# Optimization experiments

Hardware: AMD Instinct MI355X
Metric: run time of the kernel (lower is better)

Reference implementation:

```python
import jax, jax.numpy as jnp
import numpy as np

B, IN, H = 8192, 512, 512


def _binarize(w):
    # sign() forward with straight-through gradient (ebnn Binarize)
    return w + jax.lax.stop_gradient(jnp.sign(w) - w)


def setup_inputs() -> dict:
    key = jax.random.key(0)
    ks = jax.random.split(key, 7)
    stdv = 1.0 / np.sqrt(H)
    return {
        "x": jax.random.normal(ks[0], (B, IN), jnp.float32),
        "hx": jax.random.normal(ks[1], (B, H), jnp.float32),
        "cx": jax.random.normal(ks[2], (B, H), jnp.float32),
        "W_ih": jax.random.uniform(ks[3], (4 * H, IN), jnp.float32, -stdv, stdv),
        "W_hh": jax.random.uniform(ks[4], (4 * H, H), jnp.float32, -stdv, stdv),
        "bias_ih": jax.random.uniform(ks[5], (4 * H,), jnp.float32, -stdv, stdv),
        "bias_hh": jax.random.uniform(ks[6], (4 * H,), jnp.float32, -stdv, stdv),
    }


def reference(x, hx, cx, W_ih, W_hh, bias_ih, bias_hh):
    # gates: [B, 4H] = x @ sign(W_ih)^T + b_ih + hx @ sign(W_hh)^T + b_hh
    gates = (jnp.einsum("bi,gi->bg", x, _binarize(W_ih)) + bias_ih
             + jnp.einsum("bh,gh->bg", hx, _binarize(W_hh)) + bias_hh)
    ingate, forgetgate, cellgate, outgate = jnp.split(gates, 4, axis=1)
    cy = jax.nn.sigmoid(forgetgate) * cx + jax.nn.sigmoid(ingate) * jnp.tanh(cellgate)
    hy = jax.nn.sigmoid(outgate) * jnp.tanh(cy)
    return (hy, cy)
```

## Files before the change

kernel.cpp:

```cpp
#include <hip/hip_runtime.h>
#include <hip/hip_bf16.h>
#include <stdint.h>


typedef __attribute__((ext_vector_type(4))) int int4x;
typedef __attribute__((ext_vector_type(4))) float float4x;

#define B_DIM 8192
#define H_DIM 512

__device__ __forceinline__ float bf2f(uint16_t u) {
  return __uint_as_float(((uint32_t)u) << 16);
}
__device__ __forceinline__ uint16_t f2bf(float f) {
  uint32_t u = __float_as_uint(f);
  return (uint16_t)((u + 0x7FFFu + ((u >> 16) & 1u)) >> 16);
}
__device__ __forceinline__ float sigm(float x) { return 1.0f / (1.0f + __expf(-x)); }
__device__ __forceinline__ float tanh_f(float x) { return 2.0f / (1.0f + __expf(-2.0f * x)) - 1.0f; }

__device__ __forceinline__ void gld_lds16(const void* g, void* l) {
  __builtin_amdgcn_global_load_lds((const __attribute__((address_space(1))) char*)g,
                                   (__attribute__((address_space(3))) char*)l, 16, 0, 0);
}

__device__ __forceinline__ int detect_f32(const void* x) {
  const int l = threadIdx.x & 63;
  uint32_t wrd = ((const uint32_t*)x)[l];
  uint32_t e0 = (wrd >> 7) & 0xFFu, e1 = (wrd >> 23) & 0xFFu;
  return __ballot(e0 > 0x85u || e1 > 0x85u) != 0ull;
}

__global__ __launch_bounds__(256) void prep_kernel(
    const void* __restrict__ x, const void* __restrict__ hx,
    const void* __restrict__ w_ih, const void* __restrict__ w_hh,
    int8_t* __restrict__ Xhi, int8_t* __restrict__ Xlo, int8_t* __restrict__ Bp) {
  const int isF32 = detect_f32(x);
  const int w = threadIdx.x >> 6, l = threadIdx.x & 63;
  const int half = l >> 5, lk = l & 31;
  if (blockIdx.x < 2048) {
    const int m = blockIdx.x * 4 + w;
    const int k = half * 512 + lk * 16;
    const void* src = half ? hx : x;
    const long soff = (long)m * 512 + lk * 16;
    float v[16];
    if (isF32) {
      const float4x* s4 = (const float4x*)((const float*)src + soff);
#pragma unroll
      for (int q = 0; q < 4; ++q) {
        float4x t = s4[q];
        v[q * 4] = t[0]; v[q * 4 + 1] = t[1]; v[q * 4 + 2] = t[2]; v[q * 4 + 3] = t[3];
      }
    } else {
      const uint16_t* s = (const uint16_t*)src + soff;
#pragma unroll
      for (int j = 0; j < 16; ++j) v[j] = bf2f(s[j]);
    }
    union { int8_t b[16]; int4x v4; } uh, ul;
#pragma unroll
    for (int j = 0; j < 16; ++j) {
      float c = fminf(fmaxf(v[j], -8.0f), 8.0f);
      int xf = __float2int_rn(c * 4096.0f);
      xf = xf > 32639 ? 32639 : xf;
      xf = xf < -32768 ? -32768 : xf;
      const int lo = (xf << 24) >> 24;
      const int hi = (xf - lo) >> 8;
      ul.b[j] = (int8_t)lo;
      uh.b[j] = (int8_t)hi;
    }
    const int tile = ((m >> 4) << 4) | (k >> 6);
    const int lit = ((l & 3) << 4) | (m & 15);
    *(int4x*)(Xhi + (long)tile * 1024 + lit * 16) = uh.v4;
    *(int4x*)(Xlo + (long)tile * 1024 + lit * 16) = ul.v4;
  } else {
    const int p = (blockIdx.x - 2048) * 4 + w;
    const int n = ((p >> 4) & 3) * 512 + ((p >> 6) << 4) + (p & 15);
    const int k = half * 512 + lk * 16;
    const void* src = half ? w_hh : w_ih;
    const long soff = (long)n * 512 + lk * 16;
    union { int8_t b[16]; int4x v4; } us;
    if (isF32) {
      const float4x* s4 = (const float4x*)((const float*)src + soff);
#pragma unroll
      for (int q = 0; q < 4; ++q) {
        float4x t = s4[q];
#pragma unroll
        for (int j = 0; j < 4; ++j) {
          const float wv = t[j];
          us.b[q * 4 + j] = (int8_t)(wv > 0.f ? 1 : (wv < 0.f ? -1 : 0));
        }
      }
    } else {
      const uint16_t* s = (const uint16_t*)src + soff;
#pragma unroll
      for (int j = 0; j < 16; ++j) {
        const uint16_t u = s[j];
        us.b[j] = (int8_t)(((u & 0x7FFFu) == 0) ? 0 : ((u & 0x8000u) ? -1 : 1));
      }
    }
    const int tile = ((p >> 4) << 4) | (k >> 6);
    const int lit = ((l & 3) << 4) | (p & 15);
    *(int4x*)(Bp + (long)tile * 1024 + lit * 16) = us.v4;
  }
}

__global__ __launch_bounds__(256, 4) void blstm_gemm_kernel(
    const int8_t* __restrict__ Xhi, const int8_t* __restrict__ Xlo,
    const int8_t* __restrict__ Bp, const void* __restrict__ b_ih,
    const void* __restrict__ b_hh, const void* __restrict__ cx,
    const void* __restrict__ xdet, void* __restrict__ out) {
  __shared__ alignas(16) char lds[40960];
  const int tid = threadIdx.x;
  const int l = tid & 63, w = tid >> 6;
  const int lrow = l & 15, lq = l >> 4;
  const int isF32 = detect_f32(xdet);
  const int bx = blockIdx.x, by = blockIdx.y;

  const int8_t* sp[5];
  int dof[5];
#pragma unroll
  for (int i = 0; i < 5; ++i) {
    const int c = w * 5 + i;
    if (c < 8) {
      sp[i] = Xhi + ((long)(by * 8 + c) * 16) * 1024 + l * 16;
      dof[i] = c * 1024;
    } else if (c < 16) {
      sp[i] = Xlo + ((long)(by * 8 + (c - 8)) * 16) * 1024 + l * 16;
      dof[i] = 8192 + (c - 8) * 1024;
    } else {
      sp[i] = Bp + ((long)(bx * 4 + (c - 16)) * 16) * 1024 + l * 16;
      dof[i] = 16384 + (c - 16) * 1024;
    }
  }

  int4x acch[2][4], accl[2][4];
#pragma unroll
  for (int mt = 0; mt < 2; ++mt)
#pragma unroll
    for (int nt = 0; nt < 4; ++nt) {
      acch[mt][nt] = (int4x){0, 0, 0, 0};
      accl[mt][nt] = (int4x){0, 0, 0, 0};
    }

#pragma unroll
  for (int i = 0; i < 5; ++i) {
    gld_lds16(sp[i], lds + dof[i]);
    sp[i] += 1024;
  }

  for (int ks = 0; ks < 16; ++ks) {
    __syncthreads();
    const char* cur = lds + (ks & 1) * 20480;
    if (ks < 15) {
      char* nb = lds + ((ks + 1) & 1) * 20480;
#pragma unroll
      for (int i = 0; i < 5; ++i) {
        gld_lds16(sp[i], nb + dof[i]);
        sp[i] += 1024;
      }
    }
    int4x ah[2], al[2], b[4];
#pragma unroll
    for (int mt = 0; mt < 2; ++mt) {
      ah[mt] = *(const int4x*)(cur + (w * 2 + mt) * 1024 + l * 16);
      al[mt] = *(const int4x*)(cur + 8192 + (w * 2 + mt) * 1024 + l * 16);
    }
#pragma unroll
    for (int nt = 0; nt < 4; ++nt)
      b[nt] = *(const int4x*)(cur + 16384 + nt * 1024 + l * 16);
#pragma unroll
    for (int mt = 0; mt < 2; ++mt)
#pragma unroll
      for (int nt = 0; nt < 4; ++nt) {
        acch[mt][nt] = __builtin_amdgcn_mfma_i32_16x16x64_i8(ah[mt], b[nt], acch[mt][nt], 0, 0, 0);
        accl[mt][nt] = __builtin_amdgcn_mfma_i32_16x16x64_i8(al[mt], b[nt], accl[mt][nt], 0, 0, 0);
      }
  }

  const long CYo = (long)B_DIM * H_DIM;
  const int c = bx * 16 + lrow;
  float biasv[4];
#pragma unroll
  for (int g = 0; g < 4; ++g) {
    if (isF32)
      biasv[g] = ((const float*)b_ih)[g * 512 + c] + ((const float*)b_hh)[g * 512 + c];
    else
      biasv[g] = bf2f(((const uint16_t*)b_ih)[g * 512 + c]) + bf2f(((const uint16_t*)b_hh)[g * 512 + c]);
  }
  float* outF = (float*)out;
  uint16_t* outB = (uint16_t*)out;
#pragma unroll
  for (int mt = 0; mt < 2; ++mt) {
#pragma unroll
    for (int r = 0; r < 4; ++r) {
      const int row = by * 128 + (w * 2 + mt) * 16 + lq * 4 + r;
      const long cidx = (long)row * H_DIM + c;
      float vg[4];
#pragma unroll
      for (int g = 0; g < 4; ++g)
        vg[g] = fmaf((float)acch[mt][g][r], 0.0625f,
                     fmaf((float)accl[mt][g][r], 2.44140625e-4f, biasv[g]));
      const float cxv = isF32 ? ((const float*)cx)[cidx] : bf2f(((const uint16_t*)cx)[cidx]);
      const float ig = sigm(vg[0]), fg = sigm(vg[1]), og = sigm(vg[3]);
      const float cg = tanh_f(vg[2]);
      const float cy = fg * cxv + ig * cg;
      const float hy = og * tanh_f(cy);
      if (isF32) {
        outF[cidx] = hy;
        outF[CYo + cidx] = cy;
      } else {
        outB[cidx] = f2bf(hy);
        outB[CYo + cidx] = f2bf(cy);
      }
    }
  }
}

extern "C" void kernel_launch(void* const* d_in, const int* in_sizes, int n_in,
                              void* d_out, int out_size, void* d_ws, size_t ws_size,
                              hipStream_t stream) {
  const void* x = d_in[0];
  const void* hx = d_in[1];
  const void* cx = d_in[2];
  const void* W_ih = d_in[3];
  const void* W_hh = d_in[4];
  const void* b_ih = d_in[5];
  const void* b_hh = d_in[6];
  char* ws = (char*)d_ws;
  int8_t* Xhi = (int8_t*)ws;
  int8_t* Xlo = (int8_t*)(ws + 8388608);
  int8_t* Bp = (int8_t*)(ws + 16777216);

  prep_kernel<<<2560, 256, 0, stream>>>(x, hx, W_ih, W_hh, Xhi, Xlo, Bp);
  dim3 grid(32, 64);
  blstm_gemm_kernel<<<grid, 256, 0, stream>>>(Xhi, Xlo, Bp, b_ih, b_hh, cx, x, d_out);
}
```

Baseline: 166.5 us.

## Widen GEMM block tile to 128x128 with 8 waves and restructure prep writes

The GEMM block now covers 32 hidden columns (128 gate columns) with 8 waves in a 4x2 arrangement, so each loaded X tile is reused across twice as many output columns. This halves the number of blocks and cuts redundant A-tile traffic, at the cost of more LDS per block and lower block-level occupancy. The prep kernel is reorganised so each block handles 16 rows across all K, writing contiguous 16-byte chunks per quad, and it uses vectorised bf16 loads, aiming for better store coalescing with fewer blocks.

After: 165.1 us. About the same (-0.8%).

```diff
diff --git a/kernel.cpp b/kernel.cpp
--- a/kernel.cpp
+++ b/kernel.cpp
@@ -5,6 +5,7 @@
 
 typedef __attribute__((ext_vector_type(4))) int int4x;
 typedef __attribute__((ext_vector_type(4))) float float4x;
+typedef __attribute__((ext_vector_type(8))) short short8;
 
 #define B_DIM 8192
 #define H_DIM 512
@@ -29,6 +30,23 @@
   uint32_t wrd = ((const uint32_t*)x)[l];
   uint32_t e0 = (wrd >> 7) & 0xFFu, e1 = (wrd >> 23) & 0xFFu;
   return __ballot(e0 > 0x85u || e1 > 0x85u) != 0ull;
+}
+
+__device__ __forceinline__ void quant16(const float* v, int4x* uh, int4x* ul) {
+  union { int8_t b[16]; int4x v4; } h, lo;
+#pragma unroll
+  for (int j = 0; j < 16; ++j) {
+    float c = fminf(fmaxf(v[j], -8.0f), 8.0f);
+    int xf = __float2int_rn(c * 4096.0f);
+    xf = xf > 32639 ? 32639 : xf;
+    xf = xf < -32768 ? -32768 : xf;
+    const int lb = (xf << 24) >> 24;
+    const int hb = (xf - lb) >> 8;
+    lo.b[j] = (int8_t)lb;
+    h.b[j] = (int8_t)hb;
+  }
+  *uh = h.v4;
+  *ul = lo.v4;
 }
 
 __global__ __launch_bounds__(256) void prep_kernel(
@@ -37,90 +55,93 @@
     int8_t* __restrict__ Xhi, int8_t* __restrict__ Xlo, int8_t* __restrict__ Bp) {
   const int isF32 = detect_f32(x);
   const int w = threadIdx.x >> 6, l = threadIdx.x & 63;
-  const int half = l >> 5, lk = l & 31;
-  if (blockIdx.x < 2048) {
-    const int m = blockIdx.x * 4 + w;
-    const int k = half * 512 + lk * 16;
-    const void* src = half ? hx : x;
-    const long soff = (long)m * 512 + lk * 16;
-    float v[16];
-    if (isF32) {
-      const float4x* s4 = (const float4x*)((const float*)src + soff);
-#pragma unroll
-      for (int q = 0; q < 4; ++q) {
-        float4x t = s4[q];
-        v[q * 4] = t[0]; v[q * 4 + 1] = t[1]; v[q * 4 + 2] = t[2]; v[q * 4 + 3] = t[3];
-      }
-    } else {
-      const uint16_t* s = (const uint16_t*)src + soff;
-#pragma unroll
-      for (int j = 0; j < 16; ++j) v[j] = bf2f(s[j]);
-    }
-    union { int8_t b[16]; int4x v4; } uh, ul;
-#pragma unroll
-    for (int j = 0; j < 16; ++j) {
-      float c = fminf(fmaxf(v[j], -8.0f), 8.0f);
-      int xf = __float2int_rn(c * 4096.0f);
-      xf = xf > 32639 ? 32639 : xf;
-      xf = xf < -32768 ? -32768 : xf;
-      const int lo = (xf << 24) >> 24;
-      const int hi = (xf - lo) >> 8;
-      ul.b[j] = (int8_t)lo;
-      uh.b[j] = (int8_t)hi;
-    }
-    const int tile = ((m >> 4) << 4) | (k >> 6);
-    const int lit = ((l & 3) << 4) | (m & 15);
-    *(int4x*)(Xhi + (long)tile * 1024 + lit * 16) = uh.v4;
-    *(int4x*)(Xlo + (long)tile * 1024 + lit * 16) = ul.v4;
+  const int rsub = w * 4 + (l & 3);
+  const int kbase = (l >> 2) * 16;
+  if (blockIdx.x < 512) {
+    const int mg = blockIdx.x;
+    const int m = mg * 16 + rsub;
+#pragma unroll
+    for (int qk = 0; qk < 4; ++qk) {
+      const int k = qk * 256 + kbase;
+      const void* src = (k < 512) ? x : hx;
+      const long soff = (long)m * 512 + (k & 511);
+      float v[16];
+      if (isF32) {
+        const float4x* s4 = (const float4x*)((const float*)src + soff);
+#pragma unroll
+        for (int q = 0; q < 4; ++q) {
+          float4x t = s4[q];
+          v[q * 4] = t[0]; v[q * 4 + 1] = t[1]; v[q * 4 + 2] = t[2]; v[q * 4 + 3] = t[3];
+        }
+      } else {
+        const short8* s8 = (const short8*)((const uint16_t*)src + soff);
+#pragma unroll
+        for (int q = 0; q < 2; ++q) {
+          short8 t = s8[q];
+#pragma unroll
+          for (int j = 0; j < 8; ++j) v[q * 8 + j] = bf2f((uint16_t)t[j]);
+        }
+      }
+      int4x uh, ul;
+      quant16(v, &uh, &ul);
+      const int kt = k >> 6, quad = (k >> 4) & 3;
+      const long off = (long)(mg * 16 + kt) * 1024 + quad * 256 + rsub * 16;
+      *(int4x*)(Xhi + off) = uh;
+      *(int4x*)(Xlo + off) = ul;
+    }
   } else {
-    const int p = (blockIdx.x - 2048) * 4 + w;
+    const int pg = blockIdx.x - 512;
+    const int p = pg * 16 + rsub;
     const int n = ((p >> 4) & 3) * 512 + ((p >> 6) << 4) + (p & 15);
-    const int k = half * 512 + lk * 16;
-    const void* src = half ? w_hh : w_ih;
-    const long soff = (long)n * 512 + lk * 16;
-    union { int8_t b[16]; int4x v4; } us;
-    if (isF32) {
-      const float4x* s4 = (const float4x*)((const float*)src + soff);
-#pragma unroll
-      for (int q = 0; q < 4; ++q) {
-        float4x t = s4[q];
-#pragma unroll
-        for (int j = 0; j < 4; ++j) {
-          const float wv = t[j];
-          us.b[q * 4 + j] = (int8_t)(wv > 0.f ? 1 : (wv < 0.f ? -1 : 0));
-        }
-      }
-    } else {
-      const uint16_t* s = (const uint16_t*)src + soff;
-#pragma unroll
-      for (int j = 0; j < 16; ++j) {
-        const uint16_t u = s[j];
-        us.b[j] = (int8_t)(((u & 0x7FFFu) == 0) ? 0 : ((u & 0x8000u) ? -1 : 1));
-      }
-    }
-    const int tile = ((p >> 4) << 4) | (k >> 6);
-    const int lit = ((l & 3) << 4) | (p & 15);
-    *(int4x*)(Bp + (long)tile * 1024 + lit * 16) = us.v4;
-  }
-}
-
-__global__ __launch_bounds__(256, 4) void blstm_gemm_kernel(
+#pragma unroll
+    for (int qk = 0; qk < 4; ++qk) {
+      const int k = qk * 256 + kbase;
+      const void* src = (k < 512) ? w_ih : w_hh;
+      const long soff = (long)n * 512 + (k & 511);
+      union { int8_t b[16]; int4x v4; } us;
+      if (isF32) {
+        const float4x* s4 = (const float4x*)((const float*)src + soff);
+#pragma unroll
+        for (int q = 0; q < 4; ++q) {
+          float4x t = s4[q];
+#pragma unroll
+          for (int j = 0; j < 4; ++j) {
+            const float wv = t[j];
+            us.b[q * 4 + j] = (int8_t)(wv > 0.f ? 1 : (wv < 0.f ? -1 : 0));
+          }
+        }
+      } else {
+        const uint16_t* s = (const uint16_t*)src + soff;
+#pragma unroll
+        for (int j = 0; j < 16; ++j) {
+          const uint16_t u = s[j];
+          us.b[j] = (int8_t)(((u & 0x7FFFu) == 0) ? 0 : ((u & 0x8000u) ? -1 : 1));
+        }
+      }
+      const int kt = k >> 6, quad = (k >> 4) & 3;
+      *(int4x*)(Bp + (long)(pg * 16 + kt) * 1024 + quad * 256 + rsub * 16) = us.v4;
+    }
+  }
+}
+
+__global__ __launch_bounds__(512, 2) void blstm_gemm_kernel(
     const int8_t* __restrict__ Xhi, const int8_t* __restrict__ Xlo,
     const int8_t* __restrict__ Bp, const void* __restrict__ b_ih,
     const void* __restrict__ b_hh, const void* __restrict__ cx,
     const void* __restrict__ xdet, void* __restrict__ out) {
-  __shared__ alignas(16) char lds[40960];
+  __shared__ alignas(16) char lds[49152];
   const int tid = threadIdx.x;
   const int l = tid & 63, w = tid >> 6;
   const int lrow = l & 15, lq = l >> 4;
+  const int wy = w >> 1, wx = w & 1;
   const int isF32 = detect_f32(xdet);
   const int bx = blockIdx.x, by = blockIdx.y;
 
-  const int8_t* sp[5];
-  int dof[5];
-#pragma unroll
-  for (int i = 0; i < 5; ++i) {
-    const int c = w * 5 + i;
+  const int8_t* sp[3];
+  int dof[3];
+#pragma unroll
+  for (int i = 0; i < 3; ++i) {
+    const int c = w * 3 + i;
     if (c < 8) {
       sp[i] = Xhi + ((long)(by * 8 + c) * 16) * 1024 + l * 16;
       dof[i] = c * 1024;
@@ -128,7 +149,7 @@
       sp[i] = Xlo + ((long)(by * 8 + (c - 8)) * 16) * 1024 + l * 16;
       dof[i] = 8192 + (c - 8) * 1024;
     } else {
-      sp[i] = Bp + ((long)(bx * 4 + (c - 16)) * 16) * 1024 + l * 16;
+      sp[i] = Bp + ((long)(bx * 8 + (c - 16)) * 16) * 1024 + l * 16;
       dof[i] = 16384 + (c - 16) * 1024;
     }
   }
@@ -137,24 +158,24 @@
 #pragma unroll
   for (int mt = 0; mt < 2; ++mt)
 #pragma unroll
-    for (int nt = 0; nt < 4; ++nt) {
-      acch[mt][nt] = (int4x){0, 0, 0, 0};
-      accl[mt][nt] = (int4x){0, 0, 0, 0};
-    }
-
-#pragma unroll
-  for (int i = 0; i < 5; ++i) {
+    for (int g = 0; g < 4; ++g) {
+      acch[mt][g] = (int4x){0, 0, 0, 0};
+      accl[mt][g] = (int4x){0, 0, 0, 0};
+    }
+
+#pragma unroll
+  for (int i = 0; i < 3; ++i) {
     gld_lds16(sp[i], lds + dof[i]);
     sp[i] += 1024;
   }
 
   for (int ks = 0; ks < 16; ++ks) {
     __syncthreads();
-    const char* cur = lds + (ks & 1) * 20480;
+    const char* cur = lds + (ks & 1) * 24576;
     if (ks < 15) {
-      char* nb = lds + ((ks + 1) & 1) * 20480;
-#pragma unroll
-      for (int i = 0; i < 5; ++i) {
+      char* nb = lds + ((ks + 1) & 1) * 24576;
+#pragma unroll
+      for (int i = 0; i < 3; ++i) {
         gld_lds16(sp[i], nb + dof[i]);
         sp[i] += 1024;
       }
@@ -162,23 +183,23 @@
     int4x ah[2], al[2], b[4];
 #pragma unroll
     for (int mt = 0; mt < 2; ++mt) {
-      ah[mt] = *(const int4x*)(cur + (w * 2 + mt) * 1024 + l * 16);
-      al[mt] = *(const int4x*)(cur + 8192 + (w * 2 + mt) * 1024 + l * 16);
-    }
-#pragma unroll
-    for (int nt = 0; nt < 4; ++nt)
-      b[nt] = *(const int4x*)(cur + 16384 + nt * 1024 + l * 16);
+      ah[mt] = *(const int4x*)(cur + (wy * 2 + mt) * 1024 + l * 16);
+      al[mt] = *(const int4x*)(cur + 8192 + (wy * 2 + mt) * 1024 + l * 16);
+    }
+#pragma unroll
+    for (int g = 0; g < 4; ++g)
+      b[g] = *(const int4x*)(cur + 16384 + (wx * 4 + g) * 1024 + l * 16);
 #pragma unroll
     for (int mt = 0; mt < 2; ++mt)
 #pragma unroll
-      for (int nt = 0; nt < 4; ++nt) {
-        acch[mt][nt] = __builtin_amdgcn_mfma_i32_16x16x64_i8(ah[mt], b[nt], acch[mt][nt], 0, 0, 0);
-        accl[mt][nt] = __builtin_amdgcn_mfma_i32_16x16x64_i8(al[mt], b[nt], accl[mt][nt], 0, 0, 0);
+      for (int g = 0; g < 4; ++g) {
+        acch[mt][g] = __builtin_amdgcn_mfma_i32_16x16x64_i8(ah[mt], b[g], acch[mt][g], 0, 0, 0);
+        accl[mt][g] = __builtin_amdgcn_mfma_i32_16x16x64_i8(al[mt], b[g], accl[mt][g], 0, 0, 0);
       }
   }
 
   const long CYo = (long)B_DIM * H_DIM;
-  const int c = bx * 16 + lrow;
+  const int c = bx * 32 + wx * 16 + lrow;
   float biasv[4];
 #pragma unroll
   for (int g = 0; g < 4; ++g) {
@@ -193,7 +214,7 @@
   for (int mt = 0; mt < 2; ++mt) {
 #pragma unroll
     for (int r = 0; r < 4; ++r) {
-      const int row = by * 128 + (w * 2 + mt) * 16 + lq * 4 + r;
+      const int row = by * 128 + wy * 32 + mt * 16 + lq * 4 + r;
       const long cidx = (long)row * H_DIM + c;
       float vg[4];
 #pragma unroll
@@ -231,7 +252,7 @@
   int8_t* Xlo = (int8_t*)(ws + 8388608);
   int8_t* Bp = (int8_t*)(ws + 16777216);
 
-  prep_kernel<<<2560, 256, 0, stream>>>(x, hx, W_ih, W_hh, Xhi, Xlo, Bp);
-  dim3 grid(32, 64);
-  blstm_gemm_kernel<<<grid, 256, 0, stream>>>(Xhi, Xlo, Bp, b_ih, b_hh, cx, x, d_out);
-}
+  prep_kernel<<<640, 256, 0, stream>>>(x, hx, W_ih, W_hh, Xhi, Xlo, Bp);
+  dim3 grid(16, 64);
+  blstm_gemm_kernel<<<grid, 512, 0, stream>>>(Xhi, Xlo, Bp, b_ih, b_hh, cx, x, d_out);
+}
```
